# Kernel optimization log

Hardware: AMD Instinct MI355X
Metric: run time of the kernel (lower is better)

## Reference

```python
import jax, jax.numpy as jnp
import numpy as np

B, C, H, W = 2, 128, 96, 96
HEADS, DHEAD, WIN = 4, 32, 5
INNER = HEADS * DHEAD
PAD = WIN // 2


def setup_inputs() -> dict:
    key = jax.random.key(0)
    k1, k2, k3, k4, k5 = jax.random.split(key, 5)
    s = 1.0 / np.sqrt(C)
    return {
        "x": jax.random.normal(k1, (B, C, H, W), dtype=jnp.float32),
        "wq": jax.random.normal(k2, (INNER, C), dtype=jnp.float32) * s,
        "wk": jax.random.normal(k3, (INNER, C), dtype=jnp.float32) * s,
        "wv": jax.random.normal(k4, (INNER, C), dtype=jnp.float32) * s,
        "wproj": jax.random.normal(k5, (C, INNER), dtype=jnp.float32) * s,
    }


def _windows(t):
    # same neighborhood ordering as F.unfold (row-major over kernel offsets).
    tp = jnp.pad(t, ((0, 0), (0, 0), (0, 0), (PAD, PAD), (PAD, PAD)))
    wins = [tp[:, :, :, di:di + H, dj:dj + W]
            for di in range(WIN) for dj in range(WIN)]
    return jnp.stack(wins, axis=3)


def reference(x, wq, wk, wv, wproj):
    # 1x1 convs == per-pixel linear maps
    q = jnp.einsum('oc,bcxy->boxy', wq, x).reshape(B, HEADS, DHEAD, H, W)
    k = jnp.einsum('oc,bcxy->boxy', wk, x).reshape(B, HEADS, DHEAD, H, W)
    v = jnp.einsum('oc,bcxy->boxy', wv, x).reshape(B, HEADS, DHEAD, H, W)

    k_win = _windows(k)  # (B,h,d,25,H,W)
    v_win = _windows(v)

    scale = 1.0 / np.sqrt(DHEAD)
    attn = jnp.einsum('bhdxy,bhdkxy->bhkxy', q, k_win) * scale
    attn = jax.nn.softmax(attn, axis=2)  # softmax over the 25 window positions
    out = jnp.einsum('bhkxy,bhdkxy->bhdxy', attn, v_win)

    out = out.reshape(B, INNER, H, W)
    return jnp.einsum('co,boxy->bcxy', wproj, out)
```

## Files before the change

kernel.cpp:

```cpp
#include <hip/hip_runtime.h>
#include <hip/hip_bf16.h>
#include <hip/hip_fp16.h>

#define PP 9216
#define OO 384

typedef _Float16 f16x8 __attribute__((ext_vector_type(8)));
typedef _Float16 h2    __attribute__((ext_vector_type(2)));
typedef float    f32x4 __attribute__((ext_vector_type(4)));

#if defined(__has_builtin)
# if __has_builtin(__builtin_amdgcn_fdot2)
#  define HAS_FDOT2 1
# endif
#endif

__device__ __forceinline__ float dot2acc(h2 a, h2 b, float c) {
#ifdef HAS_FDOT2
    return __builtin_amdgcn_fdot2(a, b, c, false);
#else
    return c + (float)a[0] * (float)b[0] + (float)a[1] * (float)b[1];
#endif
}

__global__ __launch_bounds__(256) void prep(
    const float* __restrict__ x, const float* __restrict__ wq,
    const float* __restrict__ wk, const float* __restrict__ wv,
    const float* __restrict__ wp,
    _Float16* __restrict__ xT, _Float16* __restrict__ wqkv,
    _Float16* __restrict__ wproj)
{
    const int t = threadIdx.x;
    if (blockIdx.y == 4) {
        if (blockIdx.z) return;
        int idx = blockIdx.x * 256 + t;
        if (idx < 49152) {
            int o = idx >> 7;
            const float* src = (o < 128) ? wq : ((o < 256) ? wk : wv);
            wqkv[idx] = (_Float16)src[(o & 127) * 128 + (idx & 127)];
        } else if (idx < 65536) {
            int j = idx - 49152;
            wproj[j] = (_Float16)wp[j];
        }
        return;
    }
    __shared__ float sT[32][33];
    const int p0 = blockIdx.x * 32;
    const int c0 = blockIdx.y * 32;
    const int b  = blockIdx.z;
    const int row = t >> 3, col = t & 7;

    const float* xb = x + (size_t)b * 128 * PP;
    float4 v = *(const float4*)(xb + (size_t)(c0 + row) * PP + p0 + col * 4);
    sT[col * 4 + 0][row] = v.x;
    sT[col * 4 + 1][row] = v.y;
    sT[col * 4 + 2][row] = v.z;
    sT[col * 4 + 3][row] = v.w;
    __syncthreads();

    _Float16 h[4];
    #pragma unroll
    for (int j = 0; j < 4; j++) h[j] = (_Float16)sT[row][col * 4 + j];
    *(ushort4*)(xT + (size_t)b * PP * 128 + (size_t)(p0 + row) * 128 + c0 + col * 4) =
        *(ushort4*)h;
}

__global__ __launch_bounds__(256) void qkv_gemm(
    const _Float16* __restrict__ xT, const _Float16* __restrict__ wqkv,
    _Float16* __restrict__ qkv)
{
    __shared__ _Float16 sEpi[4][32][104];

    const int b = blockIdx.z;
    const int p0 = blockIdx.x * 64;
    const int nbase = blockIdx.y * 192;
    const int t = threadIdx.x;
    const int w = t >> 6, lane = t & 63;
    const int lm = lane & 15, quad = lane >> 4;
    const int ms0 = (w & 1) * 32;
    const int nw = (w >> 1) * 96;

    const _Float16* xb = xT + (size_t)b * PP * 128;
    _Float16* qb = qkv + (size_t)b * PP * OO;

    f16x8 A[2][4];
    #pragma unroll
    for (int ms = 0; ms < 2; ms++)
        #pragma unroll
        for (int kc = 0; kc < 4; kc++)
            A[ms][kc] = *(const f16x8*)(xb + (size_t)(p0 + ms0 + ms * 16 + lm) * 128
                                        + kc * 32 + quad * 8);

    for (int nt = 0; nt < 6; nt++) {
        const int n0 = nbase + nw + nt * 16;
        f16x8 Bf[4];
        #pragma unroll
        for (int kc = 0; kc < 4; kc++)
            Bf[kc] = *(const f16x8*)(wqkv + (size_t)(n0 + lm) * 128 + kc * 32 + quad * 8);
        f32x4 acc[2];
        #pragma unroll
        for (int ms = 0; ms < 2; ms++) {
            acc[ms] = (f32x4){0.f, 0.f, 0.f, 0.f};
            #pragma unroll
            for (int kc = 0; kc < 4; kc++)
                acc[ms] = __builtin_amdgcn_mfma_f32_16x16x32_f16(A[ms][kc], Bf[kc], acc[ms], 0, 0, 0);
        }
        #pragma unroll
        for (int ms = 0; ms < 2; ms++)
            #pragma unroll
            for (int r = 0; r < 4; r++)
                sEpi[w][ms * 16 + quad * 4 + r][nt * 16 + lm] = (_Float16)acc[ms][r];
    }

    #pragma unroll
    for (int it = 0; it < 6; it++) {
        int idx = it * 64 + lane;
        int row = idx / 12;
        int ch  = idx % 12;
        uint4 v = *(const uint4*)&sEpi[w][row][ch * 8];
        *(uint4*)(qb + (size_t)(p0 + ms0 + row) * OO + nbase + nw + ch * 8) = v;
    }
}

__global__ __launch_bounds__(256) void attn2(
    const _Float16* __restrict__ qkv, _Float16* __restrict__ ao)
{
    __shared__ _Float16 sK[144 * 40];
    __shared__ _Float16 sV[144 * 40];
    __shared__ float sS[64 * 28];

    const int t = threadIdx.x;
    const int x0 = blockIdx.x * 8, y0 = blockIdx.y * 8;
    const int b = blockIdx.z >> 2, h = blockIdx.z & 3;
    const _Float16* base = qkv + (size_t)b * PP * OO;

    for (int u = t; u < 288; u += 256) {
        const int arr = (u >= 144) ? 1 : 0;
        const int pos = u - 144 * arr;
        const int gy = y0 - 2 + pos / 12;
        const int gx = x0 - 2 + pos % 12;
        _Float16* dst = (arr ? sV : sK) + pos * 40;
        if ((unsigned)gy < 96u && (unsigned)gx < 96u) {
            const _Float16* src = base + (size_t)(gy * 96 + gx) * OO + 128 + arr * 128 + h * 32;
            #pragma unroll
            for (int j = 0; j < 4; j++)
                *(uint4*)(dst + j * 8) = *(const uint4*)(src + j * 8);
        } else {
            uint4 z = {0u, 0u, 0u, 0u};
            #pragma unroll
            for (int j = 0; j < 4; j++) *(uint4*)(dst + j * 8) = z;
        }
    }

    const int px = t & 63, w = t >> 6;
    const int ly = px >> 3, lx = px & 7;
    const int gp = (y0 + ly) * 96 + x0 + lx;

    h2 qreg[16];
    {
        const _Float16* qs = base + (size_t)gp * OO + h * 32;
        #pragma unroll
        for (int j = 0; j < 4; j++)
            *(uint4*)(&qreg[j * 4]) = *(const uint4*)(qs + j * 8);
    }
    __syncthreads();

    const float scale = 0.17677669529663689f;
    for (int pos = w; pos < 25; pos += 4) {
        const int hp = (ly + pos / 5) * 12 + lx + pos % 5;
        const _Float16* kr = sK + hp * 40;
        h2 kreg[16];
        #pragma unroll
        for (int j = 0; j < 4; j++)
            *(uint4*)(&kreg[j * 4]) = *(const uint4*)(kr + j * 8);
        float s0 = 0.f, s1 = 0.f;
        #pragma unroll
        for (int j = 0; j < 8; j++) {
            s0 = dot2acc(qreg[2 * j], kreg[2 * j], s0);
            s1 = dot2acc(qreg[2 * j + 1], kreg[2 * j + 1], s1);
        }
        sS[px * 28 + pos] = (s0 + s1) * scale;
    }
    __syncthreads();

    if (t < 64) {
        float* row = sS + t * 28;
        float m = row[0];
        #pragma unroll
        for (int p = 1; p < 25; p++) m = fmaxf(m, row[p]);
        float sum = 0.f;
        float e[25];
        #pragma unroll
        for (int p = 0; p < 25; p++) { e[p] = __expf(row[p] - m); sum += e[p]; }
        const float inv = 1.f / sum;
        #pragma unroll
        for (int p = 0; p < 25; p++) row[p] = e[p] * inv;
    }
    __syncthreads();

    float at[25];
    #pragma unroll
    for (int p = 0; p < 25; p++) at[p] = sS[px * 28 + p];

    float f[8];
    #pragma unroll
    for (int j = 0; j < 8; j++) f[j] = 0.f;
    for (int p = 0; p < 25; p++) {
        const int hp = (ly + p / 5) * 12 + lx + p % 5;
        h2 vreg[4];
        *(uint4*)vreg = *(const uint4*)(sV + hp * 40 + w * 8);
        #pragma unroll
        for (int j = 0; j < 4; j++) {
            f[2 * j]     += at[p] * (float)vreg[j][0];
            f[2 * j + 1] += at[p] * (float)vreg[j][1];
        }
    }
    _Float16 ho[8];
    #pragma unroll
    for (int j = 0; j < 8; j++) ho[j] = (_Float16)f[j];
    *(uint4*)(ao + ((size_t)b * PP + gp) * 128 + h * 32 + w * 8) = *(uint4*)ho;
}

__global__ __launch_bounds__(256) void proj_gemm(
    const _Float16* __restrict__ ao, const _Float16* __restrict__ wproj,
    float* __restrict__ out)
{
    const int b = blockIdx.z;
    const int p0 = blockIdx.x * 64;
    const int t = threadIdx.x;
    const int w = t >> 6, lane = t & 63;
    const int lm = lane & 15, quad = lane >> 4;
    const int ms0 = (w & 1) * 32;
    const int nw = (w >> 1) * 64;

    const _Float16* ab = ao + (size_t)b * PP * 128;
    float* ob = out + (size_t)b * 128 * PP;

    f16x8 A[2][4];
    #pragma unroll
    for (int ms = 0; ms < 2; ms++)
        #pragma unroll
        for (int kc = 0; kc < 4; kc++)
            A[ms][kc] = *(const f16x8*)(ab + (size_t)(p0 + ms0 + ms * 16 + lm) * 128
                                        + kc * 32 + quad * 8);

    for (int nt = 0; nt < 4; nt++) {
        const int n0 = nw + nt * 16;
        f16x8 Bf[4];
        #pragma unroll
        for (int kc = 0; kc < 4; kc++)
            Bf[kc] = *(const f16x8*)(wproj + (size_t)(n0 + lm) * 128 + kc * 32 + quad * 8);
        f32x4 acc[2];
        #pragma unroll
        for (int ms = 0; ms < 2; ms++) {
            acc[ms] = (f32x4){0.f, 0.f, 0.f, 0.f};
            #pragma unroll
            for (int kc = 0; kc < 4; kc++)
                acc[ms] = __builtin_amdgcn_mfma_f32_16x16x32_f16(A[ms][kc], Bf[kc], acc[ms], 0, 0, 0);
        }
        #pragma unroll
        for (int ms = 0; ms < 2; ms++) {
            float4 v = make_float4(acc[ms][0], acc[ms][1], acc[ms][2], acc[ms][3]);
            *(float4*)(ob + (size_t)(n0 + lm) * PP + p0 + ms0 + ms * 16 + quad * 4) = v;
        }
    }
}

extern "C" void kernel_launch(void* const* d_in, const int* in_sizes, int n_in,
                              void* d_out, int out_size, void* d_ws, size_t ws_size,
                              hipStream_t stream)
{
    const float* x  = (const float*)d_in[0];
    const float* wq = (const float*)d_in[1];
    const float* wk = (const float*)d_in[2];
    const float* wv = (const float*)d_in[3];
    const float* wp = (const float*)d_in[4];
    float* out = (float*)d_out;

    _Float16* ws    = (_Float16*)d_ws;
    _Float16* xT    = ws;
    _Float16* wqkv  = xT + 2359296;
    _Float16* wproj = wqkv + 49152;
    _Float16* qkvh  = wproj + 16384;
    _Float16* aoh   = qkvh + 7077888;

    prep<<<dim3(288, 5, 2), 256, 0, stream>>>(x, wq, wk, wv, wp, xT, wqkv, wproj);
    qkv_gemm<<<dim3(144, 2, 2), 256, 0, stream>>>(xT, wqkv, qkvh);
    attn2<<<dim3(12, 12, 8), 256, 0, stream>>>(qkvh, aoh);
    proj_gemm<<<dim3(144, 1, 2), 256, 0, stream>>>(aoh, wproj, out);
}
```

Before: 107.9 us.

## Fuse fp32-to-fp16 conversion and transpose into GEMM loads, drop prep kernel

Result: slower. 118.6 us (+9.9%).

```diff
diff --git a/kernel.cpp b/kernel.cpp
--- a/kernel.cpp
+++ b/kernel.cpp
@@ -23,50 +23,18 @@
 #endif
 }
 
-__global__ __launch_bounds__(256) void prep(
+__device__ __forceinline__ f16x8 cvt8(float4 u0, float4 u1) {
+    f16x8 r;
+    r[0] = (_Float16)u0.x; r[1] = (_Float16)u0.y;
+    r[2] = (_Float16)u0.z; r[3] = (_Float16)u0.w;
+    r[4] = (_Float16)u1.x; r[5] = (_Float16)u1.y;
+    r[6] = (_Float16)u1.z; r[7] = (_Float16)u1.w;
+    return r;
+}
+
+__global__ __launch_bounds__(256) void qkv_gemm(
     const float* __restrict__ x, const float* __restrict__ wq,
     const float* __restrict__ wk, const float* __restrict__ wv,
-    const float* __restrict__ wp,
-    _Float16* __restrict__ xT, _Float16* __restrict__ wqkv,
-    _Float16* __restrict__ wproj)
-{
-    const int t = threadIdx.x;
-    if (blockIdx.y == 4) {
-        if (blockIdx.z) return;
-        int idx = blockIdx.x * 256 + t;
-        if (idx < 49152) {
-            int o = idx >> 7;
-            const float* src = (o < 128) ? wq : ((o < 256) ? wk : wv);
-            wqkv[idx] = (_Float16)src[(o & 127) * 128 + (idx & 127)];
-        } else if (idx < 65536) {
-            int j = idx - 49152;
-            wproj[j] = (_Float16)wp[j];
-        }
-        return;
-    }
-    __shared__ float sT[32][33];
-    const int p0 = blockIdx.x * 32;
-    const int c0 = blockIdx.y * 32;
-    const int b  = blockIdx.z;
-    const int row = t >> 3, col = t & 7;
-
-    const float* xb = x + (size_t)b * 128 * PP;
-    float4 v = *(const float4*)(xb + (size_t)(c0 + row) * PP + p0 + col * 4);
-    sT[col * 4 + 0][row] = v.x;
-    sT[col * 4 + 1][row] = v.y;
-    sT[col * 4 + 2][row] = v.z;
-    sT[col * 4 + 3][row] = v.w;
-    __syncthreads();
-
-    _Float16 h[4];
-    #pragma unroll
-    for (int j = 0; j < 4; j++) h[j] = (_Float16)sT[row][col * 4 + j];
-    *(ushort4*)(xT + (size_t)b * PP * 128 + (size_t)(p0 + row) * 128 + c0 + col * 4) =
-        *(ushort4*)h;
-}
-
-__global__ __launch_bounds__(256) void qkv_gemm(
-    const _Float16* __restrict__ xT, const _Float16* __restrict__ wqkv,
     _Float16* __restrict__ qkv)
 {
     __shared__ _Float16 sEpi[4][32][104];
@@ -80,23 +48,37 @@
     const int ms0 = (w & 1) * 32;
     const int nw = (w >> 1) * 96;
 
-    const _Float16* xb = xT + (size_t)b * PP * 128;
+    const float* xb = x + (size_t)b * 128 * PP;
     _Float16* qb = qkv + (size_t)b * PP * OO;
 
     f16x8 A[2][4];
     #pragma unroll
-    for (int ms = 0; ms < 2; ms++)
-        #pragma unroll
-        for (int kc = 0; kc < 4; kc++)
-            A[ms][kc] = *(const f16x8*)(xb + (size_t)(p0 + ms0 + ms * 16 + lm) * 128
-                                        + kc * 32 + quad * 8);
+    for (int ms = 0; ms < 2; ms++) {
+        const float* xp = xb + p0 + ms0 + ms * 16 + lm;
+        #pragma unroll
+        for (int kc = 0; kc < 4; kc++) {
+            const float* s = xp + (size_t)(kc * 32 + quad * 8) * PP;
+            float tmp[8];
+            #pragma unroll
+            for (int j = 0; j < 8; j++) tmp[j] = s[(size_t)j * PP];
+            #pragma unroll
+            for (int j = 0; j < 8; j++) A[ms][kc][j] = (_Float16)tmp[j];
+        }
+    }
 
     for (int nt = 0; nt < 6; nt++) {
         const int n0 = nbase + nw + nt * 16;
+        const int o = n0 + lm;
+        const float* wrow = (o < 128) ? (wq + (size_t)o * 128)
+                          : (o < 256) ? (wk + (size_t)(o - 128) * 128)
+                                      : (wv + (size_t)(o - 256) * 128);
         f16x8 Bf[4];
         #pragma unroll
-        for (int kc = 0; kc < 4; kc++)
-            Bf[kc] = *(const f16x8*)(wqkv + (size_t)(n0 + lm) * 128 + kc * 32 + quad * 8);
+        for (int kc = 0; kc < 4; kc++) {
+            float4 u0 = *(const float4*)(wrow + kc * 32 + quad * 8);
+            float4 u1 = *(const float4*)(wrow + kc * 32 + quad * 8 + 4);
+            Bf[kc] = cvt8(u0, u1);
+        }
         f32x4 acc[2];
         #pragma unroll
         for (int ms = 0; ms < 2; ms++) {
@@ -127,7 +109,7 @@
 {
     __shared__ _Float16 sK[144 * 40];
     __shared__ _Float16 sV[144 * 40];
-    __shared__ float sS[64 * 28];
+    __shared__ float sS[64 * 27];
 
     const int t = threadIdx.x;
     const int x0 = blockIdx.x * 8, y0 = blockIdx.y * 8;
@@ -179,12 +161,13 @@
             s0 = dot2acc(qreg[2 * j], kreg[2 * j], s0);
             s1 = dot2acc(qreg[2 * j + 1], kreg[2 * j + 1], s1);
         }
-        sS[px * 28 + pos] = (s0 + s1) * scale;
+        sS[px * 27 + pos] = (s0 + s1) * scale;
     }
     __syncthreads();
 
-    if (t < 64) {
-        float* row = sS + t * 28;
+    if ((t & 63) < 16) {
+        const int sp = (t >> 6) * 16 + (t & 15);
+        float* row = sS + sp * 27;
         float m = row[0];
         #pragma unroll
         for (int p = 1; p < 25; p++) m = fmaxf(m, row[p]);
@@ -200,7 +183,7 @@
 
     float at[25];
     #pragma unroll
-    for (int p = 0; p < 25; p++) at[p] = sS[px * 28 + p];
+    for (int p = 0; p < 25; p++) at[p] = sS[px * 27 + p];
 
     float f[8];
     #pragma unroll
@@ -222,47 +205,42 @@
 }
 
 __global__ __launch_bounds__(256) void proj_gemm(
-    const _Float16* __restrict__ ao, const _Float16* __restrict__ wproj,
+    const _Float16* __restrict__ ao, const float* __restrict__ wp,
     float* __restrict__ out)
 {
     const int b = blockIdx.z;
-    const int p0 = blockIdx.x * 64;
+    const int p0 = blockIdx.x * 32;
     const int t = threadIdx.x;
     const int w = t >> 6, lane = t & 63;
     const int lm = lane & 15, quad = lane >> 4;
-    const int ms0 = (w & 1) * 32;
+    const int ms0 = (w & 1) * 16;
     const int nw = (w >> 1) * 64;
 
     const _Float16* ab = ao + (size_t)b * PP * 128;
     float* ob = out + (size_t)b * 128 * PP;
 
-    f16x8 A[2][4];
-    #pragma unroll
-    for (int ms = 0; ms < 2; ms++)
-        #pragma unroll
-        for (int kc = 0; kc < 4; kc++)
-            A[ms][kc] = *(const f16x8*)(ab + (size_t)(p0 + ms0 + ms * 16 + lm) * 128
-                                        + kc * 32 + quad * 8);
-
+    f16x8 A[4];
+    #pragma unroll
+    for (int kc = 0; kc < 4; kc++)
+        A[kc] = *(const f16x8*)(ab + (size_t)(p0 + ms0 + lm) * 128 + kc * 32 + quad * 8);
+
+    #pragma unroll
     for (int nt = 0; nt < 4; nt++) {
         const int n0 = nw + nt * 16;
+        const float* wrow = wp + (size_t)(n0 + lm) * 128;
         f16x8 Bf[4];
         #pragma unroll
+        for (int kc = 0; kc < 4; kc++) {
+            float4 u0 = *(const float4*)(wrow + kc * 32 + quad * 8);
+            float4 u1 = *(const float4*)(wrow + kc * 32 + quad * 8 + 4);
+            Bf[kc] = cvt8(u0, u1);
+        }
+        f32x4 acc = (f32x4){0.f, 0.f, 0.f, 0.f};
+        #pragma unroll
         for (int kc = 0; kc < 4; kc++)
-            Bf[kc] = *(const f16x8*)(wproj + (size_t)(n0 + lm) * 128 + kc * 32 + quad * 8);
-        f32x4 acc[2];
-        #pragma unroll
-        for (int ms = 0; ms < 2; ms++) {
-            acc[ms] = (f32x4){0.f, 0.f, 0.f, 0.f};
-            #pragma unroll
-            for (int kc = 0; kc < 4; kc++)
-                acc[ms] = __builtin_amdgcn_mfma_f32_16x16x32_f16(A[ms][kc], Bf[kc], acc[ms], 0, 0, 0);
-        }
-        #pragma unroll
-        for (int ms = 0; ms < 2; ms++) {
-            float4 v = make_float4(acc[ms][0], acc[ms][1], acc[ms][2], acc[ms][3]);
-            *(float4*)(ob + (size_t)(n0 + lm) * PP + p0 + ms0 + ms * 16 + quad * 4) = v;
-        }
+            acc = __builtin_amdgcn_mfma_f32_16x16x32_f16(A[kc], Bf[kc], acc, 0, 0, 0);
+        float4 v = make_float4(acc[0], acc[1], acc[2], acc[3]);
+        *(float4*)(ob + (size_t)(n0 + lm) * PP + p0 + ms0 + quad * 4) = v;
     }
 }
 
@@ -277,15 +255,10 @@
     const float* wp = (const float*)d_in[4];
     float* out = (float*)d_out;
 
-    _Float16* ws    = (_Float16*)d_ws;
-    _Float16* xT    = ws;
-    _Float16* wqkv  = xT + 2359296;
-    _Float16* wproj = wqkv + 49152;
-    _Float16* qkvh  = wproj + 16384;
-    _Float16* aoh   = qkvh + 7077888;
-
-    prep<<<dim3(288, 5, 2), 256, 0, stream>>>(x, wq, wk, wv, wp, xT, wqkv, wproj);
-    qkv_gemm<<<dim3(144, 2, 2), 256, 0, stream>>>(xT, wqkv, qkvh);
+    _Float16* qkvh = (_Float16*)d_ws;
+    _Float16* aoh  = qkvh + 7077888;
+
+    qkv_gemm<<<dim3(144, 2, 2), 256, 0, stream>>>(x, wq, wk, wv, qkvh);
     attn2<<<dim3(12, 12, 8), 256, 0, stream>>>(qkvh, aoh);
-    proj_gemm<<<dim3(144, 1, 2), 256, 0, stream>>>(aoh, wproj, out);
-}
+    proj_gemm<<<dim3(288, 1, 2), 256, 0, stream>>>(aoh, wp, out);
+}
```
